# Kernel optimization log

Hardware: AMD Instinct MI355X
Metric: run time of the kernel (lower is better)

Reference implementation:

```python
import jax, jax.numpy as jnp
import numpy as np

B, N, D, K, H = 64, 4096, 256, 11, 512
ITERS = 5
EPS = 1e-8
LN_EPS = 1e-5  # torch LayerNorm default
SCALE = D ** -0.5


def _ln(x, w, b):
    m = jnp.mean(x, axis=-1, keepdims=True)
    v = jnp.mean(jnp.square(x - m), axis=-1, keepdims=True)
    return (x - m) * jax.lax.rsqrt(v + LN_EPS) * w + b


def setup_inputs() -> dict:
    key = jax.random.key(0)
    ks = jax.random.split(key, 16)
    s = lambda k, shp, fan: jax.random.normal(k, shp, jnp.float32) * (1.0 / np.sqrt(fan))
    return {
        "inputs": jax.random.normal(ks[0], (B, N, D), jnp.float32),
        "slots_init": jax.random.normal(ks[1], (B, K, D), jnp.float32),
        "ln_f_w": jnp.ones((D,), jnp.float32), "ln_f_b": jnp.zeros((D,), jnp.float32),
        "ln_s_w": jnp.ones((D,), jnp.float32), "ln_s_b": jnp.zeros((D,), jnp.float32),
        "ln_p_w": jnp.ones((D,), jnp.float32), "ln_p_b": jnp.zeros((D,), jnp.float32),
        "Wq": s(ks[2], (D, D), D),
        "Wk": s(ks[3], (D, D), D),
        "Wv": s(ks[4], (D, D), D),
        "W_ih": s(ks[5], (3 * D, D), D), "b_ih": jnp.zeros((3 * D,), jnp.float32),
        "W_hh": s(ks[6], (3 * D, D), D), "b_hh": jnp.zeros((3 * D,), jnp.float32),
        "W1": s(ks[7], (H, D), D), "b1": jnp.zeros((H,), jnp.float32),
        "W2": s(ks[8], (D, H), H), "b2": jnp.zeros((D,), jnp.float32),
    }


def reference(inputs, slots_init, ln_f_w, ln_f_b, ln_s_w, ln_s_b, ln_p_w, ln_p_b,
              Wq, Wk, Wv, W_ih, b_ih, W_hh, b_hh, W1, b1, W2, b2):
    x = _ln(inputs, ln_f_w, ln_f_b)              # (B, N, D)
    k = x @ Wk.T                                  # (B, N, D)
    v = x @ Wv.T                                  # (B, N, D)
    slots = slots_init                            # (B, K, D)
    for _ in range(ITERS):
        slots_prev = slots
        q = _ln(slots, ln_s_w, ln_s_b) @ Wq.T     # (B, K, D)
        dots = jnp.einsum('bid,bjd->bij', q, k) * SCALE  # (B, K, N)
        attn = jax.nn.softmax(dots, axis=1) + EPS        # softmax over slots
        attn = attn / jnp.sum(attn, axis=-1, keepdims=True)
        updates = jnp.einsum('bjd,bij->bid', v, attn)    # (B, K, D)
        # GRUCell (torch semantics)
        gi = updates @ W_ih.T + b_ih              # (B, K, 3D)
        gh = slots_prev @ W_hh.T + b_hh
        i_r, i_z, i_n = jnp.split(gi, 3, axis=-1)
        h_r, h_z, h_n = jnp.split(gh, 3, axis=-1)
        r = jax.nn.sigmoid(i_r + h_r)
        z = jax.nn.sigmoid(i_z + h_z)
        n_ = jnp.tanh(i_n + r * h_n)
        slots = (1.0 - z) * n_ + z * slots_prev
        # residual MLP
        p = _ln(slots, ln_p_w, ln_p_b)
        slots = slots + jnp.maximum(p @ W1.T + b1, 0.0) @ W2.T + b2
    return slots
```

## Files before the change

### kernel.cpp

```cpp
#include <hip/hip_runtime.h>

typedef __bf16 bf16_t;
typedef bf16_t bf16x8 __attribute__((ext_vector_type(8)));
typedef bf16_t bf16x4 __attribute__((ext_vector_type(4)));
typedef float f32x4 __attribute__((ext_vector_type(4)));

#define DEVI static __device__ __forceinline__

constexpr int BB = 64;
constexpr int NN = 4096;
constexpr int DD = 256;
constexpr int KS = 11;
constexpr int KP = 16;
constexpr int HH = 512;
constexpr float EPS_A = 1e-8f;
constexpr float LNEPS = 1e-5f;
constexpr float SCALE = 0.0625f;
constexpr int MR = BB * KP;

DEVI float wredf(float v) {
#pragma unroll
  for (int o = 32; o > 0; o >>= 1) v += __shfl_xor(v, o, 64);
  return v;
}

DEVI float sigm(float x) { return 1.f / (1.f + __expf(-x)); }

__global__ void prep_weights_k(
    const float* __restrict__ s0, const float* __restrict__ s1, const float* __restrict__ s2,
    const float* __restrict__ s3, const float* __restrict__ s4, const float* __restrict__ s5,
    const float* __restrict__ s6,
    bf16_t* d0, bf16_t* d1, bf16_t* d2, bf16_t* d3, bf16_t* d4, bf16_t* d5, bf16_t* d6) {
  int i = blockIdx.x * 256 + threadIdx.x;
  const float* s; bf16_t* d; int o;
  if      (i < 65536)  { s = s0; d = d0; o = i; }
  else if (i < 131072) { s = s1; d = d1; o = i - 65536; }
  else if (i < 196608) { s = s2; d = d2; o = i - 131072; }
  else if (i < 393216) { s = s3; d = d3; o = i - 196608; }
  else if (i < 589824) { s = s4; d = d4; o = i - 393216; }
  else if (i < 720896) { s = s5; d = d5; o = i - 589824; }
  else                 { s = s6; d = d6; o = i - 720896; }
  d[o] = (bf16_t)s[o];
}

__global__ void init_slots_k(const float* __restrict__ si, float* __restrict__ slots) {
  int i = blockIdx.x * 256 + threadIdx.x;
  int d = i & 255, row = i >> 8, b = row >> 4, k = row & 15;
  slots[i] = (k < KS) ? si[((long)b * KS + k) * DD + d] : 0.f;
}

__global__ void ln_inputs_k(const float* __restrict__ x, const float* __restrict__ w,
                            const float* __restrict__ bsk, bf16_t* __restrict__ o) {
  const int wvi = threadIdx.x >> 6, lane = threadIdx.x & 63;
  const long row = (long)blockIdx.x * 4 + wvi;
  const float4 v = ((const float4*)(x + row * DD))[lane];
  float s = v.x + v.y + v.z + v.w;
  float s2 = v.x * v.x + v.y * v.y + v.z * v.z + v.w * v.w;
  s = wredf(s); s2 = wredf(s2);
  const float mean = s * (1.f / DD);
  const float var = s2 * (1.f / DD) - mean * mean;
  const float rstd = rsqrtf(var + LNEPS);
  const float4 w4 = ((const float4*)w)[lane];
  const float4 b4 = ((const float4*)bsk)[lane];
  bf16x4 ov;
  ov[0] = (bf16_t)((v.x - mean) * rstd * w4.x + b4.x);
  ov[1] = (bf16_t)((v.y - mean) * rstd * w4.y + b4.y);
  ov[2] = (bf16_t)((v.z - mean) * rstd * w4.z + b4.z);
  ov[3] = (bf16_t)((v.w - mean) * rstd * w4.w + b4.w);
  ((bf16x4*)(o + row * DD))[lane] = ov;
}

template <int MODE>
__global__ __launch_bounds__(256) void gemm_big_k(const bf16_t* __restrict__ X,
                                                  const bf16_t* __restrict__ W,
                                                  bf16_t* __restrict__ out) {
  __shared__ bf16_t As[128 * 72];
  __shared__ bf16_t Bs[256 * 72];
  const bf16_t* Ap; const bf16_t* Bp;
  if (MODE == 0) { Ap = W + (long)blockIdx.y * 128 * DD; Bp = X + (long)blockIdx.x * 256 * DD; }
  else           { Ap = X + (long)blockIdx.x * 128 * DD; Bp = W; }
  const int tid = threadIdx.x;
  const int wvi = tid >> 6, lane = tid & 63;
  const int c = lane & 15, q = lane >> 4;
  const int mh = wvi >> 1, nh = wvi & 1;
  f32x4 acc[4][8];
#pragma unroll
  for (int a = 0; a < 4; a++)
#pragma unroll
    for (int b = 0; b < 8; b++) acc[a][b] = (f32x4){0.f, 0.f, 0.f, 0.f};
  for (int kb = 0; kb < DD; kb += 64) {
#pragma unroll
    for (int it = 0; it < 4; ++it) {
      int id = it * 256 + tid, r = id >> 3, ch = id & 7;
      *(bf16x8*)(As + r * 72 + ch * 8) = *(const bf16x8*)(Ap + (long)r * DD + kb + ch * 8);
    }
#pragma unroll
    for (int it = 0; it < 8; ++it) {
      int id = it * 256 + tid, r = id >> 3, ch = id & 7;
      *(bf16x8*)(Bs + r * 72 + ch * 8) = *(const bf16x8*)(Bp + (long)r * DD + kb + ch * 8);
    }
    __syncthreads();
#pragma unroll
    for (int ks = 0; ks < 2; ++ks) {
      bf16x8 af[4], bfr[8];
#pragma unroll
      for (int mt = 0; mt < 4; mt++)
        af[mt] = *(const bf16x8*)(As + (mh * 64 + mt * 16 + c) * 72 + ks * 32 + q * 8);
#pragma unroll
      for (int nt = 0; nt < 8; nt++)
        bfr[nt] = *(const bf16x8*)(Bs + (nh * 128 + nt * 16 + c) * 72 + ks * 32 + q * 8);
#pragma unroll
      for (int mt = 0; mt < 4; mt++)
#pragma unroll
        for (int nt = 0; nt < 8; nt++)
          acc[mt][nt] = __builtin_amdgcn_mfma_f32_16x16x32_bf16(af[mt], bfr[nt], acc[mt][nt], 0, 0, 0);
    }
    __syncthreads();
  }
#pragma unroll
  for (int mt = 0; mt < 4; mt++) {
#pragma unroll
    for (int nt = 0; nt < 8; nt++) {
      bf16x4 o;
#pragma unroll
      for (int r = 0; r < 4; r++) o[r] = (bf16_t)acc[mt][nt][r];
      if (MODE == 0) {
        int dg = blockIdx.y * 128 + mh * 64 + mt * 16 + q * 4;
        long ng = (long)blockIdx.x * 256 + nh * 128 + nt * 16 + c;
        *(bf16x4*)(out + ng * DD + dg) = o;
      } else {
        long ng = (long)blockIdx.x * 128 + mh * 64 + mt * 16 + q * 4;
        int d = nh * 128 + nt * 16 + c;
        long b = ng >> 12; int nin = (int)(ng & 4095);
        *(bf16x4*)(out + (b * DD + d) * NN + nin) = o;
      }
    }
  }
}

__global__ void ln_slots_k(const float* __restrict__ slots, const float* __restrict__ lw,
                           const float* __restrict__ lb, bf16_t* __restrict__ sln,
                           bf16_t* __restrict__ spl, float* __restrict__ upd_raw,
                           float* __restrict__ rowsum) {
  const int row = blockIdx.x, d = threadIdx.x;
  upd_raw[row * DD + d] = 0.f;
  if (row < 4) rowsum[row * 256 + d] = 0.f;
  const int kk = row & 15;
  const int idx = row * DD + d;
  if (kk >= KS) { sln[idx] = (bf16_t)0.f; spl[idx] = (bf16_t)0.f; return; }
  float v = slots[idx];
  spl[idx] = (bf16_t)v;
  __shared__ float r1[4], r2[4];
  float s = wredf(v), s2 = wredf(v * v);
  const int wvi = threadIdx.x >> 6, lane = threadIdx.x & 63;
  if (lane == 0) { r1[wvi] = s; r2[wvi] = s2; }
  __syncthreads();
  float mean = (r1[0] + r1[1] + r1[2] + r1[3]) * (1.f / DD);
  float var = (r2[0] + r2[1] + r2[2] + r2[3]) * (1.f / DD) - mean * mean;
  float rstd = rsqrtf(var + LNEPS);
  sln[idx] = (bf16_t)((v - mean) * rstd * lw[d] + lb[d]);
}

template <bool BIASF, bool RELUF, bool RESF, int OUTM>
__global__ void small_gemm_k(const bf16_t* __restrict__ A, const bf16_t* __restrict__ W,
                             const float* __restrict__ bias, const float* __restrict__ res,
                             void* __restrict__ out, int C, int Kd) {
  const int lane = threadIdx.x & 63, c = lane & 15, q = lane >> 4;
  const int wid = blockIdx.x * 4 + (threadIdx.x >> 6);
  const int nct = C >> 4;
  const int mt = wid / nct, ct = wid % nct;
  const bf16_t* ap = A + (long)(mt * 16 + c) * Kd + q * 8;
  const bf16_t* wp = W + (long)(ct * 16 + c) * Kd + q * 8;
  f32x4 acc = (f32x4){0.f, 0.f, 0.f, 0.f};
  for (int k0 = 0; k0 < Kd; k0 += 32)
    acc = __builtin_amdgcn_mfma_f32_16x16x32_bf16(*(const bf16x8*)(ap + k0),
                                                  *(const bf16x8*)(wp + k0), acc, 0, 0, 0);
  const int col = ct * 16 + c;
  const float bv = BIASF ? bias[col] : 0.f;
#pragma unroll
  for (int r = 0; r < 4; r++) {
    const int row = mt * 16 + q * 4 + r;
    float v = acc[r] + bv;
    if (RELUF) v = fmaxf(v, 0.f);
    if (RESF) v += res[(long)row * C + col];
    if (OUTM == 0) ((float*)out)[(long)row * C + col] = v;
    else if (OUTM == 1) ((bf16_t*)out)[(long)row * C + col] = (bf16_t)v;
    else {
      int b = row >> 4, k2 = row & 15;
      if (k2 < KS) ((float*)out)[((long)b * KS + k2) * C + col] = v;
    }
  }
}

__global__ void dots_k(const bf16_t* __restrict__ qb, const bf16_t* __restrict__ kb,
                       float* __restrict__ dots) {
  const int b = blockIdx.x >> 3, strip = blockIdx.x & 7;
  const int wvi = threadIdx.x >> 6, lane = threadIdx.x & 63, c = lane & 15, q = lane >> 4;
  const int n0 = strip * 512 + wvi * 128;
  const bf16_t* qp = qb + (long)b * KP * DD;
  bf16x8 af[8];
#pragma unroll
  for (int kc = 0; kc < 8; kc++) af[kc] = *(const bf16x8*)(qp + c * DD + kc * 32 + q * 8);
  const bf16_t* kp = kb + (long)b * NN * DD;
  float* dp0 = dots + (long)b * KP * NN;
#pragma unroll
  for (int nt = 0; nt < 8; nt++) {
    f32x4 acc = (f32x4){0.f, 0.f, 0.f, 0.f};
    const bf16_t* bp = kp + (long)(n0 + nt * 16 + c) * DD + q * 8;
#pragma unroll
    for (int kc = 0; kc < 8; kc++)
      acc = __builtin_amdgcn_mfma_f32_16x16x32_bf16(af[kc], *(const bf16x8*)(bp + kc * 32), acc, 0, 0, 0);
    const int n = n0 + nt * 16 + c;
#pragma unroll
    for (int r = 0; r < 4; r++) dp0[(q * 4 + r) * NN + n] = acc[r] * SCALE;
  }
}

__global__ void softmax_k(const float* __restrict__ dots, bf16_t* __restrict__ att,
                          float* __restrict__ rowsum) {
  const int b = blockIdx.x >> 4, nc = blockIdx.x & 15;
  const int n = nc * 256 + threadIdx.x;
  const float* dp = dots + (long)b * KP * NN + n;
  float v[KS];
  float mx = -1e30f;
#pragma unroll
  for (int i = 0; i < KS; i++) { v[i] = dp[i * NN]; mx = fmaxf(mx, v[i]); }
  float sum = 0.f;
#pragma unroll
  for (int i = 0; i < KS; i++) { v[i] = __expf(v[i] - mx); sum += v[i]; }
  const float inv = 1.f / sum;
  bf16_t* ap = att + (long)b * KP * NN + n;
#pragma unroll
  for (int i = 0; i < KS; i++) { v[i] = v[i] * inv + EPS_A; ap[i * NN] = (bf16_t)v[i]; }
#pragma unroll
  for (int i = KS; i < KP; i++) ap[i * NN] = (bf16_t)0.f;
  __shared__ float red[KS][4];
  const int wvi = threadIdx.x >> 6, lane = threadIdx.x & 63;
#pragma unroll
  for (int i = 0; i < KS; i++) {
    float s = wredf(v[i]);
    if (lane == 0) red[i][wvi] = s;
  }
  __syncthreads();
  if (threadIdx.x < KS) {
    float s = red[threadIdx.x][0] + red[threadIdx.x][1] + red[threadIdx.x][2] + red[threadIdx.x][3];
    atomicAdd(&rowsum[b * KP + threadIdx.x], s);
  }
}

__global__ void updates_k(const bf16_t* __restrict__ att, const bf16_t* __restrict__ vT,
                          float* __restrict__ upd) {
  const int b = blockIdx.x >> 3, ksp = blockIdx.x & 7;
  const int wvi = threadIdx.x >> 6, lane = threadIdx.x & 63, c = lane & 15, q = lane >> 4;
  const int d0 = wvi * 64;
  const bf16_t* ab = att + (long)b * KP * NN;
  const bf16_t* vb = vT + (long)b * DD * NN;
  f32x4 acc[4];
#pragma unroll
  for (int dt = 0; dt < 4; dt++) acc[dt] = (f32x4){0.f, 0.f, 0.f, 0.f};
  const int j0b = ksp * 512;
  for (int j0 = j0b; j0 < j0b + 512; j0 += 32) {
    bf16x8 a = *(const bf16x8*)(ab + c * NN + j0 + q * 8);
#pragma unroll
    for (int dt = 0; dt < 4; dt++) {
      bf16x8 bb = *(const bf16x8*)(vb + (long)(d0 + dt * 16 + c) * NN + j0 + q * 8);
      acc[dt] = __builtin_amdgcn_mfma_f32_16x16x32_bf16(a, bb, acc[dt], 0, 0, 0);
    }
  }
  float* ub = upd + (long)b * KP * DD;
#pragma unroll
  for (int dt = 0; dt < 4; dt++)
#pragma unroll
    for (int r = 0; r < 4; r++)
      atomicAdd(&ub[(q * 4 + r) * DD + d0 + dt * 16 + c], acc[dt][r]);
}

__global__ void finalize_k(const float* __restrict__ upd, const float* __restrict__ rowsum,
                           bf16_t* __restrict__ o) {
  const int i = blockIdx.x * 256 + threadIdx.x;
  const int row = i >> 8, kk = row & 15;
  float v = 0.f;
  if (kk < KS) v = upd[i] / rowsum[row];
  o[i] = (bf16_t)v;
}

__global__ void gru_ln_k(const float* __restrict__ gi, const float* __restrict__ gh,
                         const float* __restrict__ sin_, const float* __restrict__ lw,
                         const float* __restrict__ lb, float* __restrict__ sout,
                         bf16_t* __restrict__ pbf) {
  const int row = blockIdx.x, d = threadIdx.x;
  const int kk = row & 15;
  const int idx = row * DD + d;
  if (kk >= KS) { sout[idx] = 0.f; pbf[idx] = (bf16_t)0.f; return; }
  const long g = (long)row * 768;
  float r = sigm(gi[g + d] + gh[g + d]);
  float z = sigm(gi[g + 256 + d] + gh[g + 256 + d]);
  float nn = tanhf(gi[g + 512 + d] + r * gh[g + 512 + d]);
  float sp = sin_[idx];
  float s = (1.f - z) * nn + z * sp;
  sout[idx] = s;
  __shared__ float r1[4], r2[4];
  float su = wredf(s), sq = wredf(s * s);
  const int wvi = threadIdx.x >> 6, lane = threadIdx.x & 63;
  if (lane == 0) { r1[wvi] = su; r2[wvi] = sq; }
  __syncthreads();
  float mean = (r1[0] + r1[1] + r1[2] + r1[3]) * (1.f / DD);
  float var = (r2[0] + r2[1] + r2[2] + r2[3]) * (1.f / DD) - mean * mean;
  float rstd = rsqrtf(var + LNEPS);
  pbf[idx] = (bf16_t)((s - mean) * rstd * lw[d] + lb[d]);
}

extern "C" void kernel_launch(void* const* d_in, const int* in_sizes, int n_in, void* d_out,
                              int out_size, void* d_ws, size_t ws_size, hipStream_t stream) {
  (void)in_sizes; (void)n_in; (void)out_size; (void)ws_size;
  const float* inputs = (const float*)d_in[0];
  const float* slots_in = (const float*)d_in[1];
  const float* ln_f_w = (const float*)d_in[2];
  const float* ln_f_b = (const float*)d_in[3];
  const float* ln_s_w = (const float*)d_in[4];
  const float* ln_s_b = (const float*)d_in[5];
  const float* ln_p_w = (const float*)d_in[6];
  const float* ln_p_b = (const float*)d_in[7];
  const float* Wq = (const float*)d_in[8];
  const float* Wk = (const float*)d_in[9];
  const float* Wv = (const float*)d_in[10];
  const float* W_ih = (const float*)d_in[11];
  const float* b_ih = (const float*)d_in[12];
  const float* W_hh = (const float*)d_in[13];
  const float* b_hh = (const float*)d_in[14];
  const float* W1 = (const float*)d_in[15];
  const float* b1 = (const float*)d_in[16];
  const float* W2 = (const float*)d_in[17];
  const float* b2 = (const float*)d_in[18];

  char* p = (char*)d_ws;
  auto alloc = [&](size_t bytes) { char* r = p; p += (bytes + 255) & ~(size_t)255; return r; };
  bf16_t* x_bf  = (bf16_t*)alloc((size_t)BB * NN * DD * 2);
  bf16_t* k_bf  = (bf16_t*)alloc((size_t)BB * NN * DD * 2);
  bf16_t* vT_bf = (bf16_t*)alloc((size_t)BB * NN * DD * 2);
  bf16_t* Wq_bf = (bf16_t*)alloc(65536 * 2);
  bf16_t* Wk_bf = (bf16_t*)alloc(65536 * 2);
  bf16_t* Wv_bf = (bf16_t*)alloc(65536 * 2);
  bf16_t* Wih_bf = (bf16_t*)alloc(196608 * 2);
  bf16_t* Whh_bf = (bf16_t*)alloc(196608 * 2);
  bf16_t* W1_bf = (bf16_t*)alloc(131072 * 2);
  bf16_t* W2_bf = (bf16_t*)alloc(131072 * 2);
  float* slots = (float*)alloc((size_t)MR * DD * 4);
  bf16_t* sln = (bf16_t*)alloc((size_t)MR * DD * 2);
  bf16_t* spl = (bf16_t*)alloc((size_t)MR * DD * 2);
  bf16_t* q_bf = (bf16_t*)alloc((size_t)MR * DD * 2);
  float* dots = (float*)alloc((size_t)BB * KP * NN * 4);
  bf16_t* att = (bf16_t*)alloc((size_t)BB * KP * NN * 2);
  float* rowsum = (float*)alloc((size_t)MR * 4);
  float* upd_raw = (float*)alloc((size_t)MR * DD * 4);
  bf16_t* upd_bf = (bf16_t*)alloc((size_t)MR * DD * 2);
  float* gi = (float*)alloc((size_t)MR * 768 * 4);
  float* gh = (float*)alloc((size_t)MR * 768 * 4);
  bf16_t* pbf = (bf16_t*)alloc((size_t)MR * DD * 2);
  bf16_t* h1 = (bf16_t*)alloc((size_t)MR * HH * 2);

  prep_weights_k<<<3328, 256, 0, stream>>>(Wq, Wk, Wv, W_ih, W_hh, W1, W2, Wq_bf, Wk_bf, Wv_bf,
                                           Wih_bf, Whh_bf, W1_bf, W2_bf);
  init_slots_k<<<1024, 256, 0, stream>>>(slots_in, slots);
  ln_inputs_k<<<65536, 256, 0, stream>>>(inputs, ln_f_w, ln_f_b, x_bf);
  gemm_big_k<0><<<dim3(1024, 2), 256, 0, stream>>>(x_bf, Wk_bf, k_bf);
  gemm_big_k<1><<<dim3(2048, 1), 256, 0, stream>>>(x_bf, Wv_bf, vT_bf);

  for (int t = 0; t < 5; t++) {
    ln_slots_k<<<1024, 256, 0, stream>>>(slots, ln_s_w, ln_s_b, sln, spl, upd_raw, rowsum);
    small_gemm_k<false, false, false, 1><<<256, 256, 0, stream>>>(sln, Wq_bf, nullptr, nullptr, q_bf, 256, 256);
    dots_k<<<512, 256, 0, stream>>>(q_bf, k_bf, dots);
    softmax_k<<<1024, 256, 0, stream>>>(dots, att, rowsum);
    updates_k<<<512, 256, 0, stream>>>(att, vT_bf, upd_raw);
    finalize_k<<<1024, 256, 0, stream>>>(upd_raw, rowsum, upd_bf);
    small_gemm_k<true, false, false, 0><<<768, 256, 0, stream>>>(upd_bf, Wih_bf, b_ih, nullptr, gi, 768, 256);
    small_gemm_k<true, false, false, 0><<<768, 256, 0, stream>>>(spl, Whh_bf, b_hh, nullptr, gh, 768, 256);
    gru_ln_k<<<1024, 256, 0, stream>>>(gi, gh, slots, ln_p_w, ln_p_b, slots, pbf);
    small_gemm_k<true, true, false, 1><<<512, 256, 0, stream>>>(pbf, W1_bf, b1, nullptr, h1, 512, 256);
    if (t < 4)
      small_gemm_k<true, false, true, 0><<<256, 256, 0, stream>>>(h1, W2_bf, b2, slots, slots, 256, 512);
    else
      small_gemm_k<true, false, true, 2><<<256, 256, 0, stream>>>(h1, W2_bf, b2, slots, d_out, 256, 512);
  }
}
```

Measured before the change: 1.200 ms.

## Fuse dots, softmax and attention-weighted update into one flash-style kernel

Replaces the separate dots, softmax and updates kernels with a single kernel. Per wave it computes q·k tiles with MFMA, applies the slot-axis softmax in registers, stages the bf16 attention tile in LDS and multiplies it directly with vT. This removes the global round trips of the fp32 dots and bf16 attention buffers and two kernel launches per iteration. Per-wave partial updates go to a workspace reduced by finalize_k instead of using atomics. The trade-offs are 64 accumulator registers per lane and a 32-way partial-sum read in finalize.

```diff
diff --git a/kernel.cpp b/kernel.cpp
--- a/kernel.cpp
+++ b/kernel.cpp
@@ -17,6 +17,8 @@
 constexpr float LNEPS = 1e-5f;
 constexpr float SCALE = 0.0625f;
 constexpr int MR = BB * KP;
+constexpr int NSPLIT = 8;
+constexpr int ASTR = 40;
 
 DEVI float wredf(float v) {
 #pragma unroll
@@ -140,10 +142,8 @@
 
 __global__ void ln_slots_k(const float* __restrict__ slots, const float* __restrict__ lw,
                            const float* __restrict__ lb, bf16_t* __restrict__ sln,
-                           bf16_t* __restrict__ spl, float* __restrict__ upd_raw,
-                           float* __restrict__ rowsum) {
+                           bf16_t* __restrict__ spl, float* __restrict__ rowsum) {
   const int row = blockIdx.x, d = threadIdx.x;
-  upd_raw[row * DD + d] = 0.f;
   if (row < 4) rowsum[row * 256 + d] = 0.f;
   const int kk = row & 15;
   const int idx = row * DD + d;
@@ -192,95 +192,99 @@
   }
 }
 
-__global__ void dots_k(const bf16_t* __restrict__ qb, const bf16_t* __restrict__ kb,
-                       float* __restrict__ dots) {
-  const int b = blockIdx.x >> 3, strip = blockIdx.x & 7;
-  const int wvi = threadIdx.x >> 6, lane = threadIdx.x & 63, c = lane & 15, q = lane >> 4;
-  const int n0 = strip * 512 + wvi * 128;
-  const bf16_t* qp = qb + (long)b * KP * DD;
+__global__ __launch_bounds__(256) void fused_attn_k(const bf16_t* __restrict__ q_bf,
+                                                    const bf16_t* __restrict__ k_bf,
+                                                    const bf16_t* __restrict__ vT_bf,
+                                                    float* __restrict__ upd_part,
+                                                    float* __restrict__ rowsum) {
+  const int b = blockIdx.x >> 3, sp = blockIdx.x & 7;
+  const int wvi = threadIdx.x >> 6, lane = threadIdx.x & 63;
+  const int c = lane & 15, q = lane >> 4;
+
+  __shared__ bf16_t att_s[4][16 * ASTR];
+  bf16_t* as = att_s[wvi];
+
+  const bf16_t* qp = q_bf + (long)b * KP * DD;
   bf16x8 af[8];
 #pragma unroll
   for (int kc = 0; kc < 8; kc++) af[kc] = *(const bf16x8*)(qp + c * DD + kc * 32 + q * 8);
-  const bf16_t* kp = kb + (long)b * NN * DD;
-  float* dp0 = dots + (long)b * KP * NN;
-#pragma unroll
-  for (int nt = 0; nt < 8; nt++) {
-    f32x4 acc = (f32x4){0.f, 0.f, 0.f, 0.f};
-    const bf16_t* bp = kp + (long)(n0 + nt * 16 + c) * DD + q * 8;
-#pragma unroll
-    for (int kc = 0; kc < 8; kc++)
-      acc = __builtin_amdgcn_mfma_f32_16x16x32_bf16(af[kc], *(const bf16x8*)(bp + kc * 32), acc, 0, 0, 0);
-    const int n = n0 + nt * 16 + c;
-#pragma unroll
-    for (int r = 0; r < 4; r++) dp0[(q * 4 + r) * NN + n] = acc[r] * SCALE;
-  }
-}
-
-__global__ void softmax_k(const float* __restrict__ dots, bf16_t* __restrict__ att,
-                          float* __restrict__ rowsum) {
-  const int b = blockIdx.x >> 4, nc = blockIdx.x & 15;
-  const int n = nc * 256 + threadIdx.x;
-  const float* dp = dots + (long)b * KP * NN + n;
-  float v[KS];
-  float mx = -1e30f;
-#pragma unroll
-  for (int i = 0; i < KS; i++) { v[i] = dp[i * NN]; mx = fmaxf(mx, v[i]); }
-  float sum = 0.f;
-#pragma unroll
-  for (int i = 0; i < KS; i++) { v[i] = __expf(v[i] - mx); sum += v[i]; }
-  const float inv = 1.f / sum;
-  bf16_t* ap = att + (long)b * KP * NN + n;
-#pragma unroll
-  for (int i = 0; i < KS; i++) { v[i] = v[i] * inv + EPS_A; ap[i * NN] = (bf16_t)v[i]; }
-#pragma unroll
-  for (int i = KS; i < KP; i++) ap[i * NN] = (bf16_t)0.f;
-  __shared__ float red[KS][4];
-  const int wvi = threadIdx.x >> 6, lane = threadIdx.x & 63;
-#pragma unroll
-  for (int i = 0; i < KS; i++) {
-    float s = wredf(v[i]);
-    if (lane == 0) red[i][wvi] = s;
-  }
-  __syncthreads();
-  if (threadIdx.x < KS) {
-    float s = red[threadIdx.x][0] + red[threadIdx.x][1] + red[threadIdx.x][2] + red[threadIdx.x][3];
-    atomicAdd(&rowsum[b * KP + threadIdx.x], s);
-  }
-}
-
-__global__ void updates_k(const bf16_t* __restrict__ att, const bf16_t* __restrict__ vT,
-                          float* __restrict__ upd) {
-  const int b = blockIdx.x >> 3, ksp = blockIdx.x & 7;
-  const int wvi = threadIdx.x >> 6, lane = threadIdx.x & 63, c = lane & 15, q = lane >> 4;
-  const int d0 = wvi * 64;
-  const bf16_t* ab = att + (long)b * KP * NN;
-  const bf16_t* vb = vT + (long)b * DD * NN;
-  f32x4 acc[4];
-#pragma unroll
-  for (int dt = 0; dt < 4; dt++) acc[dt] = (f32x4){0.f, 0.f, 0.f, 0.f};
-  const int j0b = ksp * 512;
-  for (int j0 = j0b; j0 < j0b + 512; j0 += 32) {
-    bf16x8 a = *(const bf16x8*)(ab + c * NN + j0 + q * 8);
-#pragma unroll
-    for (int dt = 0; dt < 4; dt++) {
-      bf16x8 bb = *(const bf16x8*)(vb + (long)(d0 + dt * 16 + c) * NN + j0 + q * 8);
-      acc[dt] = __builtin_amdgcn_mfma_f32_16x16x32_bf16(a, bb, acc[dt], 0, 0, 0);
-    }
-  }
-  float* ub = upd + (long)b * KP * DD;
-#pragma unroll
-  for (int dt = 0; dt < 4; dt++)
-#pragma unroll
-    for (int r = 0; r < 4; r++)
-      atomicAdd(&ub[(q * 4 + r) * DD + d0 + dt * 16 + c], acc[dt][r]);
-}
-
-__global__ void finalize_k(const float* __restrict__ upd, const float* __restrict__ rowsum,
+
+  f32x4 pacc[16];
+#pragma unroll
+  for (int dt = 0; dt < 16; dt++) pacc[dt] = (f32x4){0.f, 0.f, 0.f, 0.f};
+  float rs[4] = {0.f, 0.f, 0.f, 0.f};
+
+  const int n_base = sp * (NN / NSPLIT) + wvi * 128;
+  const bf16_t* kp = k_bf + (long)b * NN * DD;
+  const bf16_t* vp = vT_bf + (long)b * DD * NN;
+
+  for (int ch = 0; ch < 4; ++ch) {
+    const int n0 = n_base + ch * 32;
+    float v[2][4];
+#pragma unroll
+    for (int t = 0; t < 2; t++) {
+      f32x4 dacc = (f32x4){0.f, 0.f, 0.f, 0.f};
+      const bf16_t* bp = kp + (long)(n0 + t * 16 + c) * DD + q * 8;
+#pragma unroll
+      for (int kc = 0; kc < 8; kc++)
+        dacc = __builtin_amdgcn_mfma_f32_16x16x32_bf16(af[kc], *(const bf16x8*)(bp + kc * 32),
+                                                       dacc, 0, 0, 0);
+#pragma unroll
+      for (int r = 0; r < 4; r++) {
+        float dv = dacc[r] * SCALE;
+        if (q * 4 + r >= KS) dv = -1e30f;
+        v[t][r] = dv;
+      }
+      float m4 = fmaxf(fmaxf(v[t][0], v[t][1]), fmaxf(v[t][2], v[t][3]));
+      m4 = fmaxf(m4, __shfl_xor(m4, 16, 64));
+      m4 = fmaxf(m4, __shfl_xor(m4, 32, 64));
+      float s4 = 0.f;
+#pragma unroll
+      for (int r = 0; r < 4; r++) { v[t][r] = __expf(v[t][r] - m4); s4 += v[t][r]; }
+      s4 += __shfl_xor(s4, 16, 64);
+      s4 += __shfl_xor(s4, 32, 64);
+      const float inv = 1.f / s4;
+#pragma unroll
+      for (int r = 0; r < 4; r++) {
+        float a = v[t][r] * inv + EPS_A;
+        rs[r] += a;
+        as[(q * 4 + r) * ASTR + t * 16 + c] = (bf16_t)a;
+      }
+    }
+    bf16x8 pa = *(const bf16x8*)(as + c * ASTR + q * 8);
+#pragma unroll
+    for (int dt = 0; dt < 16; dt++) {
+      const bf16_t* bp2 = vp + (long)(dt * 16 + c) * NN + n0 + q * 8;
+      pacc[dt] = __builtin_amdgcn_mfma_f32_16x16x32_bf16(pa, *(const bf16x8*)(bp2),
+                                                         pacc[dt], 0, 0, 0);
+    }
+  }
+
+#pragma unroll
+  for (int off = 1; off < 16; off <<= 1)
+#pragma unroll
+    for (int r = 0; r < 4; r++) rs[r] += __shfl_xor(rs[r], off, 64);
+  if (c == 0) {
+#pragma unroll
+    for (int r = 0; r < 4; r++) atomicAdd(&rowsum[b * KP + q * 4 + r], rs[r]);
+  }
+
+  float* up = upd_part + ((long)blockIdx.x * 4 + wvi) * (KP * DD);
+#pragma unroll
+  for (int dt = 0; dt < 16; dt++)
+#pragma unroll
+    for (int r = 0; r < 4; r++) up[(q * 4 + r) * DD + dt * 16 + c] = pacc[dt][r];
+}
+
+__global__ void finalize_k(const float* __restrict__ upd_part, const float* __restrict__ rowsum,
                            bf16_t* __restrict__ o) {
   const int i = blockIdx.x * 256 + threadIdx.x;
-  const int row = i >> 8, kk = row & 15;
-  float v = 0.f;
-  if (kk < KS) v = upd[i] / rowsum[row];
+  const int row = i >> 8, d = i & 255, b = row >> 4, kk = row & 15;
+  const float* up = upd_part + (long)b * 32 * (KP * DD) + kk * DD + d;
+  float s = 0.f;
+#pragma unroll
+  for (int w = 0; w < 32; w++) s += up[(long)w * (KP * DD)];
+  float v = (kk < KS) ? s / rowsum[row] : 0.f;
   o[i] = (bf16_t)v;
 }
 
@@ -349,10 +353,8 @@
   bf16_t* sln = (bf16_t*)alloc((size_t)MR * DD * 2);
   bf16_t* spl = (bf16_t*)alloc((size_t)MR * DD * 2);
   bf16_t* q_bf = (bf16_t*)alloc((size_t)MR * DD * 2);
-  float* dots = (float*)alloc((size_t)BB * KP * NN * 4);
-  bf16_t* att = (bf16_t*)alloc((size_t)BB * KP * NN * 2);
+  float* upd_part = (float*)alloc((size_t)BB * 32 * KP * DD * 4);
   float* rowsum = (float*)alloc((size_t)MR * 4);
-  float* upd_raw = (float*)alloc((size_t)MR * DD * 4);
   bf16_t* upd_bf = (bf16_t*)alloc((size_t)MR * DD * 2);
   float* gi = (float*)alloc((size_t)MR * 768 * 4);
   float* gh = (float*)alloc((size_t)MR * 768 * 4);
@@ -367,12 +369,10 @@
   gemm_big_k<1><<<dim3(2048, 1), 256, 0, stream>>>(x_bf, Wv_bf, vT_bf);
 
   for (int t = 0; t < 5; t++) {
-    ln_slots_k<<<1024, 256, 0, stream>>>(slots, ln_s_w, ln_s_b, sln, spl, upd_raw, rowsum);
+    ln_slots_k<<<1024, 256, 0, stream>>>(slots, ln_s_w, ln_s_b, sln, spl, rowsum);
     small_gemm_k<false, false, false, 1><<<256, 256, 0, stream>>>(sln, Wq_bf, nullptr, nullptr, q_bf, 256, 256);
-    dots_k<<<512, 256, 0, stream>>>(q_bf, k_bf, dots);
-    softmax_k<<<1024, 256, 0, stream>>>(dots, att, rowsum);
-    updates_k<<<512, 256, 0, stream>>>(att, vT_bf, upd_raw);
-    finalize_k<<<1024, 256, 0, stream>>>(upd_raw, rowsum, upd_bf);
+    fused_attn_k<<<BB * NSPLIT, 256, 0, stream>>>(q_bf, k_bf, vT_bf, upd_part, rowsum);
+    finalize_k<<<1024, 256, 0, stream>>>(upd_part, rowsum, upd_bf);
     small_gemm_k<true, false, false, 0><<<768, 256, 0, stream>>>(upd_bf, Wih_bf, b_ih, nullptr, gi, 768, 256);
     small_gemm_k<true, false, false, 0><<<768, 256, 0, stream>>>(spl, Whh_bf, b_hh, nullptr, gh, 768, 256);
     gru_ln_k<<<1024, 256, 0, stream>>>(gi, gh, slots, ln_p_w, ln_p_b, slots, pbf);
```

Result: no change. 1.209 ms (+0.7%).
